# Optimization experiments

Measured on AMD Instinct MI355X. Metric: run time of the kernel, lower is better.

The kernel has to match this reference:

```python
import jax, jax.numpy as jnp
import numpy as np

N_NODES = 100000
N_EDGES = 1600000
N_GRAPHS = 512
IN_F, HID, OUT_F = 50, 128, 4


def _linear_params(key, fan_in, fan_out, bias=True):
    k1, k2 = jax.random.split(key)
    bound = 1.0 / np.sqrt(fan_in)
    W = jax.random.uniform(k1, (fan_out, fan_in), minval=-bound, maxval=bound, dtype=jnp.float32)
    if bias:
        b = jax.random.uniform(k2, (fan_out,), minval=-bound, maxval=bound, dtype=jnp.float32)
        return W, b
    return W, None


def setup_inputs() -> dict:
    key = jax.random.key(0)
    ks = jax.random.split(key, 12)
    x = jax.random.normal(ks[0], (N_NODES, IN_F), dtype=jnp.float32)
    edge_index = jax.random.randint(ks[1], (2, N_EDGES), 0, N_NODES, dtype=jnp.int32)
    batch = jnp.sort(jax.random.randint(ks[2], (N_NODES,), 0, N_GRAPHS, dtype=jnp.int32))
    # GraphConv params: lin_rel (with bias) applied to aggregated msgs, lin_root (no bias)
    W_rel1, b_rel1 = _linear_params(ks[3], IN_F, HID)
    W_root1, _ = _linear_params(ks[4], IN_F, HID, bias=False)
    W_rel2, b_rel2 = _linear_params(ks[5], HID, HID)
    W_root2, _ = _linear_params(ks[6], HID, HID, bias=False)
    W_rel3, b_rel3 = _linear_params(ks[7], HID, HID)
    W_root3, _ = _linear_params(ks[8], HID, HID, bias=False)
    W_lin, b_lin = _linear_params(ks[9], HID, OUT_F)
    return dict(x=x, edge_index=edge_index, batch=batch,
                W_rel1=W_rel1, b_rel1=b_rel1, W_root1=W_root1,
                W_rel2=W_rel2, b_rel2=b_rel2, W_root2=W_root2,
                W_rel3=W_rel3, b_rel3=b_rel3, W_root3=W_root3,
                W_lin=W_lin, b_lin=b_lin)


def _graph_conv(x, src, dst, W_rel, b_rel, W_root):
    # sum-aggregate neighbor features into target nodes, then two linears
    agg = jax.ops.segment_sum(x[src], dst, num_segments=N_NODES)  # [N, F_in]
    return agg @ W_rel.T + b_rel + x @ W_root.T


def reference(x, edge_index, batch,
              W_rel1, b_rel1, W_root1,
              W_rel2, b_rel2, W_root2,
              W_rel3, b_rel3, W_root3,
              W_lin, b_lin):
    src, dst = edge_index[0], edge_index[1]
    h = jax.nn.relu(_graph_conv(x, src, dst, W_rel1, b_rel1, W_root1))
    h = jax.nn.relu(_graph_conv(h, src, dst, W_rel2, b_rel2, W_root2))
    h = _graph_conv(h, src, dst, W_rel3, b_rel3, W_root3)
    # global mean pool over graphs
    sums = jax.ops.segment_sum(h, batch, num_segments=N_GRAPHS)  # [G, HID]
    counts = jax.ops.segment_sum(jnp.ones((N_NODES,), h.dtype), batch, num_segments=N_GRAPHS)
    pooled = sums / jnp.maximum(counts, 1.0)[:, None]
    # dropout is identity in eval mode
    return pooled @ W_lin.T + b_lin
```

## Files before the change

kernel.cpp:

```cpp
#include <hip/hip_runtime.h>
#include <hip/hip_bf16.h>
#include <stdint.h>

#define N_NODES 100000
#define N_EDGES 1600000
#define N_GRAPHS 512
#define IN_F 50
#define HID 128

#define NPART 64
#define PART_NODES ((N_NODES + NPART - 1) / NPART)
#define BCAP 28000

typedef __attribute__((ext_vector_type(8))) short bf16x8;
typedef __attribute__((ext_vector_type(4))) float f32x4;

__device__ __forceinline__ float bf2f(unsigned short s) {
    return __uint_as_float(((unsigned)s) << 16);
}
__device__ __forceinline__ unsigned short f2bf(float f) {
    unsigned u = __float_as_uint(f);
    u = (u + 0x7FFFu + ((u >> 16) & 1u)) >> 16;
    return (unsigned short)u;
}

#define PREP_W2 (N_NODES * 64)
#define PREP_W0 (NPART + 1)
#define PREP_W1 (128 * 64 + 128 * 128)
#define PREP_W3 (N_GRAPHS + 1)
#define PREP_TOTAL (PREP_W2 + PREP_W0 + PREP_W1 + PREP_W3)

__global__ __launch_bounds__(256) void prep_all(
    const float* __restrict__ x, unsigned short* __restrict__ xbf,
    int* __restrict__ bucket_cnt, int* __restrict__ rowptr,
    const float* __restrict__ Wr1, const float* __restrict__ Wo1,
    const float* __restrict__ Wr2, const float* __restrict__ Wo2,
    const float* __restrict__ Wr3, const float* __restrict__ Wo3,
    unsigned short* __restrict__ o_r1, unsigned short* __restrict__ o_o1,
    unsigned short* __restrict__ o_r2, unsigned short* __restrict__ o_o2,
    unsigned short* __restrict__ o_r3, unsigned short* __restrict__ o_o3,
    const int* __restrict__ batch, int* __restrict__ gstart) {
    int idx = blockIdx.x * 256 + threadIdx.x;
    if (idx < PREP_W2) {
        int n = idx >> 6, c = idx & 63;
        float v = (c < IN_F) ? x[(size_t)n * IN_F + c] : 0.f;
        xbf[idx] = f2bf(v);
        return;
    }
    idx -= PREP_W2;
    if (idx < PREP_W0) {
        if (idx < NPART) bucket_cnt[idx] = 0;
        else rowptr[N_NODES] = N_EDGES;
        return;
    }
    idx -= PREP_W0;
    if (idx < PREP_W1) {
        if (idx < 128 * 64) {
            int n = idx >> 6, k = idx & 63;
            unsigned short a = 0, b = 0;
            if (k < IN_F) { a = f2bf(Wr1[n * IN_F + k]); b = f2bf(Wo1[n * IN_F + k]); }
            o_r1[idx] = a; o_o1[idx] = b;
        } else {
            int i2 = idx - 128 * 64;
            o_r2[i2] = f2bf(Wr2[i2]); o_o2[i2] = f2bf(Wo2[i2]);
            o_r3[i2] = f2bf(Wr3[i2]); o_o3[i2] = f2bf(Wo3[i2]);
        }
        return;
    }
    idx -= PREP_W1;
    if (idx < PREP_W3) {
        if (idx == N_GRAPHS) { gstart[idx] = N_NODES; return; }
        int lo = 0, hi = N_NODES;
        while (lo < hi) { int m = (lo + hi) >> 1; if (batch[m] < idx) lo = m + 1; else hi = m; }
        gstart[idx] = lo;
    }
}

#define B1_BLOCKS 256
#define B1_EPT ((N_EDGES + B1_BLOCKS * 256 - 1) / (B1_BLOCKS * 256))

__global__ __launch_bounds__(256) void bucket_scatter(const int* __restrict__ src,
                                                      const int* __restrict__ dst,
                                                      int* __restrict__ bucket_cnt,
                                                      unsigned* __restrict__ pairs) {
    __shared__ int cnt[NPART], base[NPART];
    int t = threadIdx.x;
    for (int i = t; i < NPART; i += 256) cnt[i] = 0;
    __syncthreads();
    const int blockStart = blockIdx.x * (256 * B1_EPT);
    int kk[B1_EPT];
    unsigned ww[B1_EPT];
#pragma unroll
    for (int i = 0; i < B1_EPT; i++) {
        int e = blockStart + i * 256 + t;
        if (e < N_EDGES) {
            int d = dst[e];
            int k = d / PART_NODES;
            int local = d - k * PART_NODES;
            kk[i] = k;
            ww[i] = ((unsigned)src[e] << 11) | (unsigned)local;
            atomicAdd(&cnt[k], 1);
        } else kk[i] = -1;
    }
    __syncthreads();
    for (int i = t; i < NPART; i += 256) { base[i] = atomicAdd(&bucket_cnt[i], cnt[i]); cnt[i] = 0; }
    __syncthreads();
#pragma unroll
    for (int i = 0; i < B1_EPT; i++) {
        int k = kk[i];
        if (k >= 0) {
            int p = base[k] + atomicAdd(&cnt[k], 1);
            pairs[(size_t)k * BCAP + p] = ww[i];
        }
    }
}

#define LCSR_T 512
#define LCH ((PART_NODES + LCSR_T - 1) / LCSR_T)

__global__ __launch_bounds__(LCSR_T) void local_csr(const int* __restrict__ bucket_cnt,
                                                    const unsigned* __restrict__ pairs,
                                                    int* __restrict__ rowptr,
                                                    int* __restrict__ csr_src) {
    __shared__ int cur[PART_NODES];
    __shared__ int red[LCSR_T];
    __shared__ int pb[NPART];
    const int p = blockIdx.x, t = threadIdx.x;
    const int cnt = bucket_cnt[p];
    const unsigned* bp = pairs + (size_t)p * BCAP;
    const int plo = p * PART_NODES;

    for (int i = t; i < PART_NODES; i += LCSR_T) cur[i] = 0;
    if (t < NPART) pb[t] = bucket_cnt[t];
    __syncthreads();
    if (t == 0) {
        int s = 0;
        for (int i = 0; i < NPART; i++) { int v = pb[i]; pb[i] = s; s += v; }
    }
    for (int i = t; i < cnt; i += LCSR_T) atomicAdd(&cur[bp[i] & 2047u], 1);
    __syncthreads();
    const int pbase = pb[p];
    int e[LCH];
    int s = 0;
#pragma unroll
    for (int i = 0; i < LCH; i++) {
        int idx = t * LCH + i;
        e[i] = (idx < PART_NODES) ? cur[idx] : 0;
        s += e[i];
    }
    red[t] = s;
    __syncthreads();
    for (int o = 1; o < LCSR_T; o <<= 1) {
        int u = (t >= o) ? red[t - o] : 0;
        __syncthreads();
        red[t] += u;
        __syncthreads();
    }
    int run = red[t] - s;
#pragma unroll
    for (int i = 0; i < LCH; i++) {
        int idx = t * LCH + i;
        if (idx < PART_NODES) {
            cur[idx] = run;
            int node = plo + idx;
            if (node < N_NODES) rowptr[node] = pbase + run;
            run += e[i];
        }
    }
    __syncthreads();
    for (int i = t; i < cnt; i += LCSR_T) {
        unsigned v = bp[i];
        int pos = pbase + atomicAdd(&cur[v & 2047u], 1);
        csr_src[pos] = (int)(v >> 11);
    }
}

__global__ __launch_bounds__(256) void gather_x64(const unsigned short* __restrict__ xbf,
                                                  const int* __restrict__ rowptr,
                                                  const int* __restrict__ csr_src,
                                                  unsigned short* __restrict__ aggbf) {
    int gid = blockIdx.x * 256 + threadIdx.x;
    int n = gid >> 4;
    int c = threadIdx.x & 15;
    if (n >= N_NODES) return;
    int jb = rowptr[n], je = rowptr[n + 1];
    const uint2* hu = reinterpret_cast<const uint2*>(xbf);
    float a0 = 0.f, a1 = 0.f, a2 = 0.f, a3 = 0.f;
    int j = jb;
    for (; j + 3 < je; j += 4) {
        int s0 = csr_src[j], s1 = csr_src[j + 1], s2 = csr_src[j + 2], s3 = csr_src[j + 3];
        uint2 v0 = hu[(size_t)s0 * 16 + c];
        uint2 v1 = hu[(size_t)s1 * 16 + c];
        uint2 v2 = hu[(size_t)s2 * 16 + c];
        uint2 v3 = hu[(size_t)s3 * 16 + c];
        a0 += (bf2f(v0.x & 0xFFFF) + bf2f(v1.x & 0xFFFF)) + (bf2f(v2.x & 0xFFFF) + bf2f(v3.x & 0xFFFF));
        a1 += (bf2f(v0.x >> 16) + bf2f(v1.x >> 16)) + (bf2f(v2.x >> 16) + bf2f(v3.x >> 16));
        a2 += (bf2f(v0.y & 0xFFFF) + bf2f(v1.y & 0xFFFF)) + (bf2f(v2.y & 0xFFFF) + bf2f(v3.y & 0xFFFF));
        a3 += (bf2f(v0.y >> 16) + bf2f(v1.y >> 16)) + (bf2f(v2.y >> 16) + bf2f(v3.y >> 16));
    }
    for (; j < je; j++) {
        int s0 = csr_src[j];
        uint2 v0 = hu[(size_t)s0 * 16 + c];
        a0 += bf2f(v0.x & 0xFFFF);
        a1 += bf2f(v0.x >> 16);
        a2 += bf2f(v0.y & 0xFFFF);
        a3 += bf2f(v0.y >> 16);
    }
    uint2 pk;
    pk.x = (unsigned)f2bf(a0) | ((unsigned)f2bf(a1) << 16);
    pk.y = (unsigned)f2bf(a2) | ((unsigned)f2bf(a3) << 16);
    reinterpret_cast<uint2*>(aggbf)[(size_t)n * 16 + c] = pk;
}

__global__ __launch_bounds__(256) void gather_bf128(const unsigned short* __restrict__ h,
                                                    const int* __restrict__ rowptr,
                                                    const int* __restrict__ csr_src,
                                                    unsigned short* __restrict__ aggbf) {
    int gid = blockIdx.x * 256 + threadIdx.x;
    int n = gid >> 5;
    int c = threadIdx.x & 31;
    if (n >= N_NODES) return;
    int jb = rowptr[n], je = rowptr[n + 1];
    const uint2* hu = reinterpret_cast<const uint2*>(h);
    float a0 = 0.f, a1 = 0.f, a2 = 0.f, a3 = 0.f;
    int j = jb;
    for (; j + 3 < je; j += 4) {
        int s0 = csr_src[j], s1 = csr_src[j + 1], s2 = csr_src[j + 2], s3 = csr_src[j + 3];
        uint2 v0 = hu[(size_t)s0 * 32 + c];
        uint2 v1 = hu[(size_t)s1 * 32 + c];
        uint2 v2 = hu[(size_t)s2 * 32 + c];
        uint2 v3 = hu[(size_t)s3 * 32 + c];
        a0 += (bf2f(v0.x & 0xFFFF) + bf2f(v1.x & 0xFFFF)) + (bf2f(v2.x & 0xFFFF) + bf2f(v3.x & 0xFFFF));
        a1 += (bf2f(v0.x >> 16) + bf2f(v1.x >> 16)) + (bf2f(v2.x >> 16) + bf2f(v3.x >> 16));
        a2 += (bf2f(v0.y & 0xFFFF) + bf2f(v1.y & 0xFFFF)) + (bf2f(v2.y & 0xFFFF) + bf2f(v3.y & 0xFFFF));
        a3 += (bf2f(v0.y >> 16) + bf2f(v1.y >> 16)) + (bf2f(v2.y >> 16) + bf2f(v3.y >> 16));
    }
    for (; j < je; j++) {
        int s0 = csr_src[j];
        uint2 v0 = hu[(size_t)s0 * 32 + c];
        a0 += bf2f(v0.x & 0xFFFF);
        a1 += bf2f(v0.x >> 16);
        a2 += bf2f(v0.y & 0xFFFF);
        a3 += bf2f(v0.y >> 16);
    }
    uint2 pk;
    pk.x = (unsigned)f2bf(a0) | ((unsigned)f2bf(a1) << 16);
    pk.y = (unsigned)f2bf(a2) | ((unsigned)f2bf(a3) << 16);
    reinterpret_cast<uint2*>(aggbf)[(size_t)n * 32 + c] = pk;
}

template <int K1, int K2, bool RELU>
__global__ __launch_bounds__(256) void mfma_linear(
    const unsigned short* __restrict__ A1, const unsigned short* __restrict__ A2,
    const unsigned short* __restrict__ B1, const unsigned short* __restrict__ B2,
    const float* __restrict__ bias, unsigned short* __restrict__ hout) {
    constexpr int P1 = K1 * 2 + 16;
    constexpr int P2 = K2 * 2 + 16;
    constexpr int PMAX = (P1 > P2 ? P1 : P2);
    __shared__ __align__(16) unsigned char ldsb[128 * PMAX];

    const int tid = threadIdx.x;
    const int lane = tid & 63;
    const int wave = tid >> 6;
    const int ar = lane & 15;
    const int kh = lane >> 4;
    const int m0 = blockIdx.x * 128 + wave * 32;

    f32x4 acc0[8], acc1[8];
#pragma unroll
    for (int nt = 0; nt < 8; nt++) {
        acc0[nt] = (f32x4){0.f, 0.f, 0.f, 0.f};
        acc1[nt] = (f32x4){0.f, 0.f, 0.f, 0.f};
    }

    int r0 = m0 + ar;      if (r0 > N_NODES - 1) r0 = N_NODES - 1;
    int r1 = m0 + 16 + ar; if (r1 > N_NODES - 1) r1 = N_NODES - 1;

    {
        constexpr int CPR = K1 / 8;
#pragma unroll
        for (int ci = 0; ci < 128 * CPR / 256; ci++) {
            int c = ci * 256 + tid;
            int n = c / CPR, slot = c - n * CPR;
            uint4 v = *reinterpret_cast<const uint4*>(B1 + n * K1 + slot * 8);
            *reinterpret_cast<uint4*>(&ldsb[n * P1 + slot * 16]) = v;
        }
    }
    __syncthreads();
    {
        const unsigned short* a0p = A1 + (size_t)r0 * K1 + kh * 8;
        const unsigned short* a1p = A1 + (size_t)r1 * K1 + kh * 8;
#pragma unroll
        for (int ks = 0; ks < K1 / 32; ks++) {
            bf16x8 a0 = *reinterpret_cast<const bf16x8*>(a0p + ks * 32);
            bf16x8 a1 = *reinterpret_cast<const bf16x8*>(a1p + ks * 32);
#pragma unroll
            for (int nt = 0; nt < 8; nt++) {
                bf16x8 b = *reinterpret_cast<const bf16x8*>(
                    &ldsb[(nt * 16 + ar) * P1 + ks * 64 + kh * 16]);
                acc0[nt] = __builtin_amdgcn_mfma_f32_16x16x32_bf16(b, a0, acc0[nt], 0, 0, 0);
                acc1[nt] = __builtin_amdgcn_mfma_f32_16x16x32_bf16(b, a1, acc1[nt], 0, 0, 0);
            }
        }
    }
    __syncthreads();
    {
        constexpr int CPR = K2 / 8;
#pragma unroll
        for (int ci = 0; ci < 128 * CPR / 256; ci++) {
            int c = ci * 256 + tid;
            int n = c / CPR, slot = c - n * CPR;
            uint4 v = *reinterpret_cast<const uint4*>(B2 + n * K2 + slot * 8);
            *reinterpret_cast<uint4*>(&ldsb[n * P2 + slot * 16]) = v;
        }
    }
    __syncthreads();
    {
        const unsigned short* a0p = A2 + (size_t)r0 * K2 + kh * 8;
        const unsigned short* a1p = A2 + (size_t)r1 * K2 + kh * 8;
#pragma unroll
        for (int ks = 0; ks < K2 / 32; ks++) {
            bf16x8 a0 = *reinterpret_cast<const bf16x8*>(a0p + ks * 32);
            bf16x8 a1 = *reinterpret_cast<const bf16x8*>(a1p + ks * 32);
#pragma unroll
            for (int nt = 0; nt < 8; nt++) {
                bf16x8 b = *reinterpret_cast<const bf16x8*>(
                    &ldsb[(nt * 16 + ar) * P2 + ks * 64 + kh * 16]);
                acc0[nt] = __builtin_amdgcn_mfma_f32_16x16x32_bf16(b, a0, acc0[nt], 0, 0, 0);
                acc1[nt] = __builtin_amdgcn_mfma_f32_16x16x32_bf16(b, a1, acc1[nt], 0, 0, 0);
            }
        }
    }

    float4 bv[8];
#pragma unroll
    for (int nt = 0; nt < 8; nt++)
        bv[nt] = *reinterpret_cast<const float4*>(bias + nt * 16 + kh * 4);

    int node0 = m0 + ar;
    int node1 = m0 + 16 + ar;
    if (node0 < N_NODES) {
#pragma unroll
        for (int nt = 0; nt < 8; nt++) {
            float v0 = acc0[nt][0] + bv[nt].x;
            float v1 = acc0[nt][1] + bv[nt].y;
            float v2 = acc0[nt][2] + bv[nt].z;
            float v3 = acc0[nt][3] + bv[nt].w;
            if (RELU) { v0 = fmaxf(v0, 0.f); v1 = fmaxf(v1, 0.f); v2 = fmaxf(v2, 0.f); v3 = fmaxf(v3, 0.f); }
            uint2 pk;
            pk.x = (unsigned)f2bf(v0) | ((unsigned)f2bf(v1) << 16);
            pk.y = (unsigned)f2bf(v2) | ((unsigned)f2bf(v3) << 16);
            *reinterpret_cast<uint2*>(hout + (size_t)node0 * HID + nt * 16 + kh * 4) = pk;
        }
    }
    if (node1 < N_NODES) {
#pragma unroll
        for (int nt = 0; nt < 8; nt++) {
            float v0 = acc1[nt][0] + bv[nt].x;
            float v1 = acc1[nt][1] + bv[nt].y;
            float v2 = acc1[nt][2] + bv[nt].z;
            float v3 = acc1[nt][3] + bv[nt].w;
            if (RELU) { v0 = fmaxf(v0, 0.f); v1 = fmaxf(v1, 0.f); v2 = fmaxf(v2, 0.f); v3 = fmaxf(v3, 0.f); }
            uint2 pk;
            pk.x = (unsigned)f2bf(v0) | ((unsigned)f2bf(v1) << 16);
            pk.y = (unsigned)f2bf(v2) | ((unsigned)f2bf(v3) << 16);
            *reinterpret_cast<uint2*>(hout + (size_t)node1 * HID + nt * 16 + kh * 4) = pk;
        }
    }
}

__global__ __launch_bounds__(256) void pool_final(const unsigned short* __restrict__ h3,
                                                  const int* __restrict__ gstart,
                                                  const float* __restrict__ W_lin,
                                                  const float* __restrict__ b_lin,
                                                  float* __restrict__ out) {
    __shared__ float pp[4][HID];
    int g = blockIdx.x, t = threadIdx.x;
    int wave = t >> 6, lane = t & 63;
    int s0 = gstart[g], s1 = gstart[g + 1];
    const unsigned* h3u = reinterpret_cast<const unsigned*>(h3);
    float a0 = 0.f, a1 = 0.f;
    for (int n = s0 + wave; n < s1; n += 4) {
        unsigned v = h3u[(size_t)n * 64 + lane];
        a0 += bf2f((unsigned short)(v & 0xFFFF));
        a1 += bf2f((unsigned short)(v >> 16));
    }
    pp[wave][2 * lane] = a0;
    pp[wave][2 * lane + 1] = a1;
    __syncthreads();
    if (wave == 0) {
        float c = fmaxf((float)(s1 - s0), 1.f);
        float r0 = ((pp[0][2 * lane] + pp[1][2 * lane]) + (pp[2][2 * lane] + pp[3][2 * lane])) / c;
        float r1 = ((pp[0][2 * lane + 1] + pp[1][2 * lane + 1]) + (pp[2][2 * lane + 1] + pp[3][2 * lane + 1])) / c;
        pp[0][2 * lane] = r0;
        pp[0][2 * lane + 1] = r1;
    }
    __syncthreads();
    if (t < 4) {
        float s = b_lin[t];
#pragma unroll 8
        for (int k = 0; k < HID; k++) s += pp[0][k] * W_lin[t * HID + k];
        out[g * 4 + t] = s;
    }
}

extern "C" void kernel_launch(void* const* d_in, const int* in_sizes, int n_in,
                              void* d_out, int out_size, void* d_ws, size_t ws_size,
                              hipStream_t stream) {
    (void)in_sizes; (void)n_in; (void)out_size; (void)ws_size;
    const float* x      = (const float*)d_in[0];
    const int*   ei     = (const int*)d_in[1];
    const int*   batch  = (const int*)d_in[2];
    const float* W_rel1 = (const float*)d_in[3];
    const float* b_rel1 = (const float*)d_in[4];
    const float* W_root1= (const float*)d_in[5];
    const float* W_rel2 = (const float*)d_in[6];
    const float* b_rel2 = (const float*)d_in[7];
    const float* W_root2= (const float*)d_in[8];
    const float* W_rel3 = (const float*)d_in[9];
    const float* b_rel3 = (const float*)d_in[10];
    const float* W_root3= (const float*)d_in[11];
    const float* W_lin  = (const float*)d_in[12];
    const float* b_lin  = (const float*)d_in[13];
    const int* src = ei;
    const int* dst = ei + N_EDGES;

    char* ws = (char*)d_ws;
    size_t off = 0;
    auto alloc = [&](size_t bytes) { void* p = ws + off; off += (bytes + 255) & ~(size_t)255; return p; };
    unsigned short* aggbf    = (unsigned short*)alloc((size_t)N_NODES * HID * 2);
    unsigned short* h1       = (unsigned short*)alloc((size_t)N_NODES * HID * 2);
    unsigned short* xbf      = (unsigned short*)alloc((size_t)N_NODES * 64 * 2);
    int*            rowptr   = (int*)alloc((size_t)(N_NODES + 1) * 4);
    int*            csr_src  = (int*)alloc((size_t)N_EDGES * 4);
    unsigned*       pairs    = (unsigned*)alloc((size_t)NPART * BCAP * 4);
    int*            bucket_cnt = (int*)alloc(NPART * 4);
    int*            gstart   = (int*)alloc((size_t)(N_GRAPHS + 1) * 4);
    unsigned short* Wb_rel1  = (unsigned short*)alloc(128 * 64 * 2);
    unsigned short* Wb_root1 = (unsigned short*)alloc(128 * 64 * 2);
    unsigned short* Wb_rel2  = (unsigned short*)alloc(128 * 128 * 2);
    unsigned short* Wb_root2 = (unsigned short*)alloc(128 * 128 * 2);
    unsigned short* Wb_rel3  = (unsigned short*)alloc(128 * 128 * 2);
    unsigned short* Wb_root3 = (unsigned short*)alloc(128 * 128 * 2);

    prep_all<<<(PREP_TOTAL + 255) / 256, 256, 0, stream>>>(
        x, xbf, bucket_cnt, rowptr, W_rel1, W_root1, W_rel2, W_root2, W_rel3, W_root3,
        Wb_rel1, Wb_root1, Wb_rel2, Wb_root2, Wb_rel3, Wb_root3, batch, gstart);

    bucket_scatter<<<B1_BLOCKS, 256, 0, stream>>>(src, dst, bucket_cnt, pairs);
    local_csr<<<NPART, LCSR_T, 0, stream>>>(bucket_cnt, pairs, rowptr, csr_src);

    const int MFMA_BLOCKS = (N_NODES + 127) / 128;

    gather_x64<<<(N_NODES * 16 + 255) / 256, 256, 0, stream>>>(xbf, rowptr, csr_src, aggbf);
    mfma_linear<64, 64, true><<<MFMA_BLOCKS, 256, 0, stream>>>(
        aggbf, xbf, Wb_rel1, Wb_root1, b_rel1, h1);

    gather_bf128<<<(N_NODES * 32 + 255) / 256, 256, 0, stream>>>(h1, rowptr, csr_src, aggbf);
    mfma_linear<128, 128, true><<<MFMA_BLOCKS, 256, 0, stream>>>(
        aggbf, h1, Wb_rel2, Wb_root2, b_rel2, h1);

    gather_bf128<<<(N_NODES * 32 + 255) / 256, 256, 0, stream>>>(h1, rowptr, csr_src, aggbf);
    mfma_linear<128, 128, false><<<MFMA_BLOCKS, 256, 0, stream>>>(
        aggbf, h1, Wb_rel3, Wb_root3, b_rel3, aggbf);

    pool_final<<<N_GRAPHS, 256, 0, stream>>>(aggbf, gstart, W_lin, b_lin, (float*)d_out);
}
```

Before: 399.6 us.

## Fuse neighbor gather into MFMA linear kernel and use finer CSR partitions

Each GraphConv layer now runs as one kernel that sums neighbor features for a 128-node tile into LDS and then applies the rel and root MFMA matmuls. The aggregated bf16 buffer no longer makes a round trip through global memory, and three kernel launches go away. Weights are now read straight from global memory instead of being staged in LDS. The CSR build uses 256 partitions instead of 64, with 9-bit local indices, more scatter blocks and smaller local_csr blocks. The risks are lower gather parallelism per block, since each thread walks several nodes in sequence, and repeated uncached weight loads.

```diff
diff --git a/kernel.cpp b/kernel.cpp
--- a/kernel.cpp
+++ b/kernel.cpp
@@ -8,9 +8,10 @@
 #define IN_F 50
 #define HID 128
 
-#define NPART 64
+#define NPART 256
 #define PART_NODES ((N_NODES + NPART - 1) / NPART)
-#define BCAP 28000
+#define BCAP 7600
+#define LBITS 9
 
 typedef __attribute__((ext_vector_type(8))) short bf16x8;
 typedef __attribute__((ext_vector_type(4))) float f32x4;
@@ -76,7 +77,7 @@
     }
 }
 
-#define B1_BLOCKS 256
+#define B1_BLOCKS 512
 #define B1_EPT ((N_EDGES + B1_BLOCKS * 256 - 1) / (B1_BLOCKS * 256))
 
 __global__ __launch_bounds__(256) void bucket_scatter(const int* __restrict__ src,
@@ -98,7 +99,7 @@
             int k = d / PART_NODES;
             int local = d - k * PART_NODES;
             kk[i] = k;
-            ww[i] = ((unsigned)src[e] << 11) | (unsigned)local;
+            ww[i] = ((unsigned)src[e] << LBITS) | (unsigned)local;
             atomicAdd(&cnt[k], 1);
         } else kk[i] = -1;
     }
@@ -115,7 +116,7 @@
     }
 }
 
-#define LCSR_T 512
+#define LCSR_T 256
 #define LCH ((PART_NODES + LCSR_T - 1) / LCSR_T)
 
 __global__ __launch_bounds__(LCSR_T) void local_csr(const int* __restrict__ bucket_cnt,
@@ -137,7 +138,7 @@
         int s = 0;
         for (int i = 0; i < NPART; i++) { int v = pb[i]; pb[i] = s; s += v; }
     }
-    for (int i = t; i < cnt; i += LCSR_T) atomicAdd(&cur[bp[i] & 2047u], 1);
+    for (int i = t; i < cnt; i += LCSR_T) atomicAdd(&cur[bp[i] & ((1u << LBITS) - 1u)], 1);
     __syncthreads();
     const int pbase = pb[p];
     int e[LCH];
@@ -170,101 +171,65 @@
     __syncthreads();
     for (int i = t; i < cnt; i += LCSR_T) {
         unsigned v = bp[i];
-        int pos = pbase + atomicAdd(&cur[v & 2047u], 1);
-        csr_src[pos] = (int)(v >> 11);
-    }
-}
-
-__global__ __launch_bounds__(256) void gather_x64(const unsigned short* __restrict__ xbf,
-                                                  const int* __restrict__ rowptr,
-                                                  const int* __restrict__ csr_src,
-                                                  unsigned short* __restrict__ aggbf) {
-    int gid = blockIdx.x * 256 + threadIdx.x;
-    int n = gid >> 4;
-    int c = threadIdx.x & 15;
-    if (n >= N_NODES) return;
-    int jb = rowptr[n], je = rowptr[n + 1];
-    const uint2* hu = reinterpret_cast<const uint2*>(xbf);
-    float a0 = 0.f, a1 = 0.f, a2 = 0.f, a3 = 0.f;
-    int j = jb;
-    for (; j + 3 < je; j += 4) {
-        int s0 = csr_src[j], s1 = csr_src[j + 1], s2 = csr_src[j + 2], s3 = csr_src[j + 3];
-        uint2 v0 = hu[(size_t)s0 * 16 + c];
-        uint2 v1 = hu[(size_t)s1 * 16 + c];
-        uint2 v2 = hu[(size_t)s2 * 16 + c];
-        uint2 v3 = hu[(size_t)s3 * 16 + c];
-        a0 += (bf2f(v0.x & 0xFFFF) + bf2f(v1.x & 0xFFFF)) + (bf2f(v2.x & 0xFFFF) + bf2f(v3.x & 0xFFFF));
-        a1 += (bf2f(v0.x >> 16) + bf2f(v1.x >> 16)) + (bf2f(v2.x >> 16) + bf2f(v3.x >> 16));
-        a2 += (bf2f(v0.y & 0xFFFF) + bf2f(v1.y & 0xFFFF)) + (bf2f(v2.y & 0xFFFF) + bf2f(v3.y & 0xFFFF));
-        a3 += (bf2f(v0.y >> 16) + bf2f(v1.y >> 16)) + (bf2f(v2.y >> 16) + bf2f(v3.y >> 16));
-    }
-    for (; j < je; j++) {
-        int s0 = csr_src[j];
-        uint2 v0 = hu[(size_t)s0 * 16 + c];
-        a0 += bf2f(v0.x & 0xFFFF);
-        a1 += bf2f(v0.x >> 16);
-        a2 += bf2f(v0.y & 0xFFFF);
-        a3 += bf2f(v0.y >> 16);
-    }
-    uint2 pk;
-    pk.x = (unsigned)f2bf(a0) | ((unsigned)f2bf(a1) << 16);
-    pk.y = (unsigned)f2bf(a2) | ((unsigned)f2bf(a3) << 16);
-    reinterpret_cast<uint2*>(aggbf)[(size_t)n * 16 + c] = pk;
-}
-
-__global__ __launch_bounds__(256) void gather_bf128(const unsigned short* __restrict__ h,
-                                                    const int* __restrict__ rowptr,
-                                                    const int* __restrict__ csr_src,
-                                                    unsigned short* __restrict__ aggbf) {
-    int gid = blockIdx.x * 256 + threadIdx.x;
-    int n = gid >> 5;
-    int c = threadIdx.x & 31;
-    if (n >= N_NODES) return;
-    int jb = rowptr[n], je = rowptr[n + 1];
-    const uint2* hu = reinterpret_cast<const uint2*>(h);
-    float a0 = 0.f, a1 = 0.f, a2 = 0.f, a3 = 0.f;
-    int j = jb;
-    for (; j + 3 < je; j += 4) {
-        int s0 = csr_src[j], s1 = csr_src[j + 1], s2 = csr_src[j + 2], s3 = csr_src[j + 3];
-        uint2 v0 = hu[(size_t)s0 * 32 + c];
-        uint2 v1 = hu[(size_t)s1 * 32 + c];
-        uint2 v2 = hu[(size_t)s2 * 32 + c];
-        uint2 v3 = hu[(size_t)s3 * 32 + c];
-        a0 += (bf2f(v0.x & 0xFFFF) + bf2f(v1.x & 0xFFFF)) + (bf2f(v2.x & 0xFFFF) + bf2f(v3.x & 0xFFFF));
-        a1 += (bf2f(v0.x >> 16) + bf2f(v1.x >> 16)) + (bf2f(v2.x >> 16) + bf2f(v3.x >> 16));
-        a2 += (bf2f(v0.y & 0xFFFF) + bf2f(v1.y & 0xFFFF)) + (bf2f(v2.y & 0xFFFF) + bf2f(v3.y & 0xFFFF));
-        a3 += (bf2f(v0.y >> 16) + bf2f(v1.y >> 16)) + (bf2f(v2.y >> 16) + bf2f(v3.y >> 16));
-    }
-    for (; j < je; j++) {
-        int s0 = csr_src[j];
-        uint2 v0 = hu[(size_t)s0 * 32 + c];
-        a0 += bf2f(v0.x & 0xFFFF);
-        a1 += bf2f(v0.x >> 16);
-        a2 += bf2f(v0.y & 0xFFFF);
-        a3 += bf2f(v0.y >> 16);
-    }
-    uint2 pk;
-    pk.x = (unsigned)f2bf(a0) | ((unsigned)f2bf(a1) << 16);
-    pk.y = (unsigned)f2bf(a2) | ((unsigned)f2bf(a3) << 16);
-    reinterpret_cast<uint2*>(aggbf)[(size_t)n * 32 + c] = pk;
-}
-
-template <int K1, int K2, bool RELU>
-__global__ __launch_bounds__(256) void mfma_linear(
-    const unsigned short* __restrict__ A1, const unsigned short* __restrict__ A2,
+        int pos = pbase + atomicAdd(&cur[v & ((1u << LBITS) - 1u)], 1);
+        csr_src[pos] = (int)(v >> LBITS);
+    }
+}
+
+template <int K, bool RELU>
+__global__ __launch_bounds__(256) void fused_layer(
+    const unsigned short* __restrict__ hsrc,
+    const int* __restrict__ rowptr, const int* __restrict__ csr_src,
     const unsigned short* __restrict__ B1, const unsigned short* __restrict__ B2,
     const float* __restrict__ bias, unsigned short* __restrict__ hout) {
-    constexpr int P1 = K1 * 2 + 16;
-    constexpr int P2 = K2 * 2 + 16;
-    constexpr int PMAX = (P1 > P2 ? P1 : P2);
-    __shared__ __align__(16) unsigned char ldsb[128 * PMAX];
-
+    constexpr int PITCH = K * 2 + 16;
+    __shared__ __align__(16) unsigned char atile[128 * PITCH];
     const int tid = threadIdx.x;
+    const int m0 = blockIdx.x * 128;
+
+    {
+        constexpr int CL = K / 4;
+        constexpr int NG = 256 / CL;
+        constexpr int NPG = 128 / NG;
+        const int grp = tid / CL, c = tid % CL;
+        const uint2* hu = reinterpret_cast<const uint2*>(hsrc);
+        for (int ni = 0; ni < NPG; ni++) {
+            int nl = grp * NPG + ni;
+            int n = m0 + nl; if (n > N_NODES - 1) n = N_NODES - 1;
+            int jb = rowptr[n], je = rowptr[n + 1];
+            float a0 = 0.f, a1 = 0.f, a2 = 0.f, a3 = 0.f;
+            int j = jb;
+            for (; j + 3 < je; j += 4) {
+                int s0 = csr_src[j], s1 = csr_src[j + 1], s2 = csr_src[j + 2], s3 = csr_src[j + 3];
+                uint2 v0 = hu[(size_t)s0 * CL + c];
+                uint2 v1 = hu[(size_t)s1 * CL + c];
+                uint2 v2 = hu[(size_t)s2 * CL + c];
+                uint2 v3 = hu[(size_t)s3 * CL + c];
+                a0 += (bf2f(v0.x & 0xFFFF) + bf2f(v1.x & 0xFFFF)) + (bf2f(v2.x & 0xFFFF) + bf2f(v3.x & 0xFFFF));
+                a1 += (bf2f(v0.x >> 16) + bf2f(v1.x >> 16)) + (bf2f(v2.x >> 16) + bf2f(v3.x >> 16));
+                a2 += (bf2f(v0.y & 0xFFFF) + bf2f(v1.y & 0xFFFF)) + (bf2f(v2.y & 0xFFFF) + bf2f(v3.y & 0xFFFF));
+                a3 += (bf2f(v0.y >> 16) + bf2f(v1.y >> 16)) + (bf2f(v2.y >> 16) + bf2f(v3.y >> 16));
+            }
+            for (; j < je; j++) {
+                int s0 = csr_src[j];
+                uint2 v0 = hu[(size_t)s0 * CL + c];
+                a0 += bf2f(v0.x & 0xFFFF);
+                a1 += bf2f(v0.x >> 16);
+                a2 += bf2f(v0.y & 0xFFFF);
+                a3 += bf2f(v0.y >> 16);
+            }
+            uint2 pk;
+            pk.x = (unsigned)f2bf(a0) | ((unsigned)f2bf(a1) << 16);
+            pk.y = (unsigned)f2bf(a2) | ((unsigned)f2bf(a3) << 16);
+            *reinterpret_cast<uint2*>(&atile[nl * PITCH + c * 8]) = pk;
+        }
+    }
+    __syncthreads();
+
     const int lane = tid & 63;
     const int wave = tid >> 6;
     const int ar = lane & 15;
     const int kh = lane >> 4;
-    const int m0 = blockIdx.x * 128 + wave * 32;
 
     f32x4 acc0[8], acc1[8];
 #pragma unroll
@@ -273,72 +238,44 @@
         acc1[nt] = (f32x4){0.f, 0.f, 0.f, 0.f};
     }
 
-    int r0 = m0 + ar;      if (r0 > N_NODES - 1) r0 = N_NODES - 1;
-    int r1 = m0 + 16 + ar; if (r1 > N_NODES - 1) r1 = N_NODES - 1;
-
+#pragma unroll
+    for (int ks = 0; ks < K / 32; ks++) {
+        bf16x8 a0 = *reinterpret_cast<const bf16x8*>(
+            &atile[(wave * 32 + ar) * PITCH + ks * 64 + kh * 16]);
+        bf16x8 a1 = *reinterpret_cast<const bf16x8*>(
+            &atile[(wave * 32 + 16 + ar) * PITCH + ks * 64 + kh * 16]);
+#pragma unroll
+        for (int nt = 0; nt < 8; nt++) {
+            bf16x8 b = *reinterpret_cast<const bf16x8*>(B1 + (size_t)(nt * 16 + ar) * K + ks * 32 + kh * 8);
+            acc0[nt] = __builtin_amdgcn_mfma_f32_16x16x32_bf16(b, a0, acc0[nt], 0, 0, 0);
+            acc1[nt] = __builtin_amdgcn_mfma_f32_16x16x32_bf16(b, a1, acc1[nt], 0, 0, 0);
+        }
+    }
     {
-        constexpr int CPR = K1 / 8;
-#pragma unroll
-        for (int ci = 0; ci < 128 * CPR / 256; ci++) {
-            int c = ci * 256 + tid;
-            int n = c / CPR, slot = c - n * CPR;
-            uint4 v = *reinterpret_cast<const uint4*>(B1 + n * K1 + slot * 8);
-            *reinterpret_cast<uint4*>(&ldsb[n * P1 + slot * 16]) = v;
-        }
-    }
-    __syncthreads();
-    {
-        const unsigned short* a0p = A1 + (size_t)r0 * K1 + kh * 8;
-        const unsigned short* a1p = A1 + (size_t)r1 * K1 + kh * 8;
-#pragma unroll
-        for (int ks = 0; ks < K1 / 32; ks++) {
+        int r0 = m0 + wave * 32 + ar;      if (r0 > N_NODES - 1) r0 = N_NODES - 1;
+        int r1 = m0 + wave * 32 + 16 + ar; if (r1 > N_NODES - 1) r1 = N_NODES - 1;
+        const unsigned short* a0p = hsrc + (size_t)r0 * K + kh * 8;
+        const unsigned short* a1p = hsrc + (size_t)r1 * K + kh * 8;
+#pragma unroll
+        for (int ks = 0; ks < K / 32; ks++) {
             bf16x8 a0 = *reinterpret_cast<const bf16x8*>(a0p + ks * 32);
             bf16x8 a1 = *reinterpret_cast<const bf16x8*>(a1p + ks * 32);
 #pragma unroll
             for (int nt = 0; nt < 8; nt++) {
-                bf16x8 b = *reinterpret_cast<const bf16x8*>(
-                    &ldsb[(nt * 16 + ar) * P1 + ks * 64 + kh * 16]);
+                bf16x8 b = *reinterpret_cast<const bf16x8*>(B2 + (size_t)(nt * 16 + ar) * K + ks * 32 + kh * 8);
                 acc0[nt] = __builtin_amdgcn_mfma_f32_16x16x32_bf16(b, a0, acc0[nt], 0, 0, 0);
                 acc1[nt] = __builtin_amdgcn_mfma_f32_16x16x32_bf16(b, a1, acc1[nt], 0, 0, 0);
             }
         }
     }
-    __syncthreads();
-    {
-        constexpr int CPR = K2 / 8;
-#pragma unroll
-        for (int ci = 0; ci < 128 * CPR / 256; ci++) {
-            int c = ci * 256 + tid;
-            int n = c / CPR, slot = c - n * CPR;
-            uint4 v = *reinterpret_cast<const uint4*>(B2 + n * K2 + slot * 8);
-            *reinterpret_cast<uint4*>(&ldsb[n * P2 + slot * 16]) = v;
-        }
-    }
-    __syncthreads();
-    {
-        const unsigned short* a0p = A2 + (size_t)r0 * K2 + kh * 8;
-        const unsigned short* a1p = A2 + (size_t)r1 * K2 + kh * 8;
-#pragma unroll
-        for (int ks = 0; ks < K2 / 32; ks++) {
-            bf16x8 a0 = *reinterpret_cast<const bf16x8*>(a0p + ks * 32);
-            bf16x8 a1 = *reinterpret_cast<const bf16x8*>(a1p + ks * 32);
-#pragma unroll
-            for (int nt = 0; nt < 8; nt++) {
-                bf16x8 b = *reinterpret_cast<const bf16x8*>(
-                    &ldsb[(nt * 16 + ar) * P2 + ks * 64 + kh * 16]);
-                acc0[nt] = __builtin_amdgcn_mfma_f32_16x16x32_bf16(b, a0, acc0[nt], 0, 0, 0);
-                acc1[nt] = __builtin_amdgcn_mfma_f32_16x16x32_bf16(b, a1, acc1[nt], 0, 0, 0);
-            }
-        }
-    }
 
     float4 bv[8];
 #pragma unroll
     for (int nt = 0; nt < 8; nt++)
         bv[nt] = *reinterpret_cast<const float4*>(bias + nt * 16 + kh * 4);
 
-    int node0 = m0 + ar;
-    int node1 = m0 + 16 + ar;
+    int node0 = m0 + wave * 32 + ar;
+    int node1 = m0 + wave * 32 + 16 + ar;
     if (node0 < N_NODES) {
 #pragma unroll
         for (int nt = 0; nt < 8; nt++) {
@@ -428,8 +365,8 @@
     char* ws = (char*)d_ws;
     size_t off = 0;
     auto alloc = [&](size_t bytes) { void* p = ws + off; off += (bytes + 255) & ~(size_t)255; return p; };
-    unsigned short* aggbf    = (unsigned short*)alloc((size_t)N_NODES * HID * 2);
     unsigned short* h1       = (unsigned short*)alloc((size_t)N_NODES * HID * 2);
+    unsigned short* h2       = (unsigned short*)alloc((size_t)N_NODES * HID * 2);
     unsigned short* xbf      = (unsigned short*)alloc((size_t)N_NODES * 64 * 2);
     int*            rowptr   = (int*)alloc((size_t)(N_NODES + 1) * 4);
     int*            csr_src  = (int*)alloc((size_t)N_EDGES * 4);
@@ -450,19 +387,14 @@
     bucket_scatter<<<B1_BLOCKS, 256, 0, stream>>>(src, dst, bucket_cnt, pairs);
     local_csr<<<NPART, LCSR_T, 0, stream>>>(bucket_cnt, pairs, rowptr, csr_src);
 
-    const int MFMA_BLOCKS = (N_NODES + 127) / 128;
-
-    gather_x64<<<(N_NODES * 16 + 255) / 256, 256, 0, stream>>>(xbf, rowptr, csr_src, aggbf);
-    mfma_linear<64, 64, true><<<MFMA_BLOCKS, 256, 0, stream>>>(
-        aggbf, xbf, Wb_rel1, Wb_root1, b_rel1, h1);
-
-    gather_bf128<<<(N_NODES * 32 + 255) / 256, 256, 0, stream>>>(h1, rowptr, csr_src, aggbf);
-    mfma_linear<128, 128, true><<<MFMA_BLOCKS, 256, 0, stream>>>(
-        aggbf, h1, Wb_rel2, Wb_root2, b_rel2, h1);
-
-    gather_bf128<<<(N_NODES * 32 + 255) / 256, 256, 0, stream>>>(h1, rowptr, csr_src, aggbf);
-    mfma_linear<128, 128, false><<<MFMA_BLOCKS, 256, 0, stream>>>(
-        aggbf, h1, Wb_rel3, Wb_root3, b_rel3, aggbf);
-
-    pool_final<<<N_GRAPHS, 256, 0, stream>>>(aggbf, gstart, W_lin, b_lin, (float*)d_out);
-}
+    const int LBLK = (N_NODES + 127) / 128;
+
+    fused_layer<64, true><<<LBLK, 256, 0, stream>>>(
+        xbf, rowptr, csr_src, Wb_rel1, Wb_root1, b_rel1, h1);
+    fused_layer<128, true><<<LBLK, 256, 0, stream>>>(
+        h1, rowptr, csr_src, Wb_rel2, Wb_root2, b_rel2, h2);
+    fused_layer<128, false><<<LBLK, 256, 0, stream>>>(
+        h2, rowptr, csr_src, Wb_rel3, Wb_root3, b_rel3, h1);
+
+    pool_final<<<N_GRAPHS, 256, 0, stream>>>(h1, gstart, W_lin, b_lin, (float*)d_out);
+}
```

After: 646.1 us. +61.7%, slower.
